# Performance work log

Measured on AMD Instinct MI355X. Metric: run time of the kernel, lower is better.

The kernel has to match this reference:

```python
import jax, jax.numpy as jnp
import numpy as np

B, L, D, H, UNITS = 64, 1024, 1024, 1024, 1024


def setup_inputs() -> dict:
    key = jax.random.key(0)
    ks = jax.random.split(key, 8)
    s = lambda fan_in: 1.0 / np.sqrt(fan_in)
    return {
        "features": jax.random.normal(ks[0], (B, L, D), jnp.float32),
        "hidden": jax.random.normal(ks[1], (B, H), jnp.float32),
        "W1": jax.random.normal(ks[2], (D, UNITS), jnp.float32) * s(D),
        "b1": jnp.zeros((UNITS,), jnp.float32),
        "W2": jax.random.normal(ks[3], (H, UNITS), jnp.float32) * s(H),
        "b2": jnp.zeros((UNITS,), jnp.float32),
        "V": jax.random.normal(ks[4], (UNITS, 1), jnp.float32) * s(UNITS),
        "bV": jnp.zeros((1,), jnp.float32),
    }


def reference(features, hidden, W1, b1, W2, b2, V, bV):
    # features: [B, L, D], hidden: [B, H]
    proj_f = jnp.einsum("bld,du->blu", features, W1) + b1          # [B, L, U]
    proj_h = (hidden @ W2 + b2)[:, None, :]                         # [B, 1, U]
    score = jnp.tanh(proj_f + proj_h)                               # [B, L, U]
    logits = jnp.einsum("blu,uo->blo", score, V) + bV               # [B, L, 1]
    attention_weights = jax.nn.softmax(logits, axis=1)              # [B, L, 1]
    context_vector = jnp.sum(attention_weights * features, axis=1)  # [B, D]
    return context_vector, attention_weights
```

## Files before the change

### kernel.cpp

```cpp
#include <hip/hip_runtime.h>
#include <hip/hip_bf16.h>
#include <stdint.h>

#define B_ 64
#define L_ 1024
#define D_ 1024
#define U_ 1024
#define M_ (B_ * L_)

__device__ __forceinline__ int swz_k(int k, int row) {
  return (k & ~31) | (((((k >> 3) & 3) ^ ((row >> 1) & 3))) << 3) | (k & 7);
}

typedef __attribute__((ext_vector_type(8))) __bf16 bf16x8;
typedef __attribute__((ext_vector_type(4))) float f32x4;
typedef __attribute__((ext_vector_type(8))) unsigned short u16x8;

__device__ __forceinline__ unsigned short f2bf(float f) {
  unsigned u = __float_as_uint(f);
  unsigned r = (u + 0x7fffu + ((u >> 16) & 1u)) >> 16;
  return (unsigned short)r;
}

__device__ __forceinline__ float bf2f(unsigned short h) {
  return __uint_as_float(((unsigned)h) << 16);
}

__device__ __forceinline__ void async_copy16(const void* gptr, void* ldsptr) {
  __builtin_amdgcn_global_load_lds(
      (const __attribute__((address_space(1))) void*)gptr,
      (__attribute__((address_space(3))) void*)ldsptr,
      16, 0, 0);
}

__global__ __launch_bounds__(256) void convert_f_bf16(
    const float4* __restrict__ src, ushort4* __restrict__ dst) {
  long i = (long)blockIdx.x * 256 + threadIdx.x;
  float4 v = src[i];
  ushort4 o;
  o.x = f2bf(v.x); o.y = f2bf(v.y); o.z = f2bf(v.z); o.w = f2bf(v.w);
  int m = (int)(i >> 8);
  int k4 = (int)(i & 255) << 2;
  int kp = swz_k(k4, m);
  dst[(((long)m << 10) + kp) >> 2] = o;
}

__global__ __launch_bounds__(256) void transpose_w1(
    const float* __restrict__ W1, unsigned short* __restrict__ W1T) {
  __shared__ float tile[32][33];
  int tx = threadIdx.x & 31, ty = threadIdx.x >> 5;
  int u0 = blockIdx.x * 32, k0 = blockIdx.y * 32;
#pragma unroll
  for (int i = ty; i < 32; i += 8) tile[i][tx] = W1[(long)(k0 + i) * U_ + u0 + tx];
  __syncthreads();
#pragma unroll
  for (int i = ty; i < 32; i += 8) {
    int u = u0 + i, k = k0 + tx;
    W1T[(long)u * D_ + swz_k(k, u)] = f2bf(tile[tx][i]);
  }
}

__global__ __launch_bounds__(256) void proj_h_kernel(
    const float* __restrict__ hidden, const float* __restrict__ W2,
    const float* __restrict__ b1, const float* __restrict__ b2,
    float* __restrict__ ph) {
  int u = blockIdx.x * 256 + threadIdx.x;
  int bbase = blockIdx.y * 8;
  int h0 = blockIdx.z * 128;
  float acc[8];
  float bias = (blockIdx.z == 0) ? (b1[u] + b2[u]) : 0.0f;
#pragma unroll
  for (int i = 0; i < 8; ++i) acc[i] = bias;
  for (int h = h0; h < h0 + 128; ++h) {
    float w = W2[(long)h * U_ + u];
#pragma unroll
    for (int i = 0; i < 8; ++i) acc[i] += hidden[(bbase + i) * 1024 + h] * w;
  }
#pragma unroll
  for (int i = 0; i < 8; ++i) atomicAdd(&ph[(bbase + i) * U_ + u], acc[i]);
}

__global__ __launch_bounds__(256, 2) void fused_score_kernel(
    const unsigned short* __restrict__ A,
    const unsigned short* __restrict__ Bt,
    const float* __restrict__ ph,
    const float* __restrict__ V,
    float* __restrict__ logits) {
  __shared__ unsigned short As[128 * 32];
  __shared__ unsigned short Bs[128 * 32];

  const int tid = threadIdx.x;
  const int wave = tid >> 6;
  const int lane = tid & 63;
  const int l15 = lane & 15;
  const int quad = lane >> 4;
  const int wm = wave >> 1;
  const int wn = wave & 1;
  const int xk = (l15 >> 1) & 3;

  const int i = blockIdx.x;
  const int mtile = ((i >> 6) << 3) + (i & 7);
  const int ntile = (i >> 3) & 7;
  const long m0 = (long)mtile * 128;
  const int n0 = ntile * 128;

  const int srow = lane >> 2;
  const int skof = (lane & 3) * 8;
  const int c0 = wave * 2;
  const unsigned short* Ab = A + (m0 + srow) * 1024 + skof;
  const unsigned short* Bb = Bt + ((long)n0 + srow) * 1024 + skof;

  f32x4 acc[4][4];
#pragma unroll
  for (int ii = 0; ii < 4; ++ii)
#pragma unroll
    for (int j = 0; j < 4; ++j) acc[ii][j] = (f32x4){0.f, 0.f, 0.f, 0.f};

  for (int k0 = 0; k0 < 1024; k0 += 32) {
#pragma unroll
    for (int cc = 0; cc < 2; ++cc) {
      const int c = c0 + cc;
      async_copy16(Ab + (long)c * 16 * 1024 + k0, &As[c * 512]);
      async_copy16(Bb + (long)c * 16 * 1024 + k0, &Bs[c * 512]);
    }
    __syncthreads();

    bf16x8 af[4], bf[4];
#pragma unroll
    for (int mi = 0; mi < 4; ++mi)
      af[mi] = *(const bf16x8*)&As[(wm * 64 + mi * 16 + l15) * 32 + ((quad ^ xk) << 3)];
#pragma unroll
    for (int ni = 0; ni < 4; ++ni)
      bf[ni] = *(const bf16x8*)&Bs[(wn * 64 + ni * 16 + l15) * 32 + ((quad ^ xk) << 3)];
#pragma unroll
    for (int mi = 0; mi < 4; ++mi)
#pragma unroll
      for (int ni = 0; ni < 4; ++ni)
        acc[mi][ni] = __builtin_amdgcn_mfma_f32_16x16x32_bf16(
            af[mi], bf[ni], acc[mi][ni], 0, 0, 0);
    __syncthreads();
  }

  const int b = (int)(m0 >> 10);
  float phv[4], vv[4];
#pragma unroll
  for (int ni = 0; ni < 4; ++ni) {
    int u = n0 + wn * 64 + ni * 16 + l15;
    phv[ni] = ph[b * U_ + u];
    vv[ni] = V[u];
  }
#pragma unroll
  for (int mi = 0; mi < 4; ++mi) {
#pragma unroll
    for (int r = 0; r < 4; ++r) {
      float part = 0.f;
#pragma unroll
      for (int ni = 0; ni < 4; ++ni) {
        float s = acc[mi][ni][r] + phv[ni];
        float t = __expf(2.0f * s);
        float th = 1.0f - 2.0f * __builtin_amdgcn_rcpf(t + 1.0f);
        part += th * vv[ni];
      }
      part += __shfl_xor(part, 1, 16);
      part += __shfl_xor(part, 2, 16);
      part += __shfl_xor(part, 4, 16);
      part += __shfl_xor(part, 8, 16);
      if (l15 == 0)
        atomicAdd(&logits[m0 + wm * 64 + mi * 16 + quad * 4 + r], part);
    }
  }
}

__global__ __launch_bounds__(256) void softmax_kernel(
    const float* __restrict__ logits, float* __restrict__ wout) {
  __shared__ float redm[4];
  __shared__ float reds[4];
  int b = blockIdx.x;
  int tid = threadIdx.x;
  int wave = tid >> 6, lane = tid & 63;
  float4 v = *(const float4*)&logits[b * 1024 + tid * 4];
  float m = fmaxf(fmaxf(v.x, v.y), fmaxf(v.z, v.w));
#pragma unroll
  for (int off = 32; off >= 1; off >>= 1) m = fmaxf(m, __shfl_xor(m, off, 64));
  if (lane == 0) redm[wave] = m;
  __syncthreads();
  m = fmaxf(fmaxf(redm[0], redm[1]), fmaxf(redm[2], redm[3]));
  float e0 = __expf(v.x - m), e1 = __expf(v.y - m);
  float e2 = __expf(v.z - m), e3 = __expf(v.w - m);
  float s = e0 + e1 + e2 + e3;
#pragma unroll
  for (int off = 32; off >= 1; off >>= 1) s += __shfl_xor(s, off, 64);
  if (lane == 0) reds[wave] = s;
  __syncthreads();
  s = reds[0] + reds[1] + reds[2] + reds[3];
  float inv = 1.0f / s;
  float4 o = {e0 * inv, e1 * inv, e2 * inv, e3 * inv};
  *(float4*)&wout[b * 1024 + tid * 4] = o;
}

__global__ __launch_bounds__(256) void context_kernel(
    const unsigned short* __restrict__ Fh, const float* __restrict__ wv,
    float* __restrict__ out) {
  int b = blockIdx.x;
  int d4 = threadIdx.x * 4;
  int l0 = blockIdx.y * 128;
  const int hi = d4 & ~31, ch = (d4 >> 3) & 3, off = d4 & 7;
  const unsigned short* fp = Fh + ((long)b * 1024 + l0) * 1024;
  const float* wp = wv + b * 1024 + l0;
  float a0 = 0.f, a1 = 0.f, a2 = 0.f, a3 = 0.f;
#pragma unroll 4
  for (int l = 0; l < 128; ++l) {
    int xr = ((l0 + l) >> 1) & 3;
    ushort4 f = *(const ushort4*)(fp + (long)l * 1024 + hi + ((ch ^ xr) << 3) + off);
    float w = wp[l];
    a0 += w * bf2f(f.x);
    a1 += w * bf2f(f.y);
    a2 += w * bf2f(f.z);
    a3 += w * bf2f(f.w);
  }
  atomicAdd(&out[b * 1024 + d4 + 0], a0);
  atomicAdd(&out[b * 1024 + d4 + 1], a1);
  atomicAdd(&out[b * 1024 + d4 + 2], a2);
  atomicAdd(&out[b * 1024 + d4 + 3], a3);
}

extern "C" void kernel_launch(void* const* d_in, const int* in_sizes, int n_in,
                              void* d_out, int out_size, void* d_ws, size_t ws_size,
                              hipStream_t stream) {
  const float* features = (const float*)d_in[0];
  const float* hidden   = (const float*)d_in[1];
  const float* W1       = (const float*)d_in[2];
  const float* b1       = (const float*)d_in[3];
  const float* W2       = (const float*)d_in[4];
  const float* b2       = (const float*)d_in[5];
  const float* V        = (const float*)d_in[6];

  char* ws = (char*)d_ws;
  unsigned short* Fh  = (unsigned short*)ws;
  unsigned short* W1T = (unsigned short*)(ws + 134217728);
  float* ph     = (float*)(ws + 134217728 + 2097152);
  float* logits = (float*)(ws + 134217728 + 2097152 + 262144);
  float* ctx  = (float*)d_out;
  float* wout = (float*)d_out + 65536;

  hipMemsetAsync(ph, 0, 262144 + 262144, stream);
  hipMemsetAsync(d_out, 0, 65536 * sizeof(float), stream);

  convert_f_bf16<<<65536, 256, 0, stream>>>((const float4*)features, (ushort4*)Fh);
  transpose_w1<<<dim3(32, 32), 256, 0, stream>>>(W1, W1T);
  proj_h_kernel<<<dim3(4, 8, 8), 256, 0, stream>>>(hidden, W2, b1, b2, ph);
  fused_score_kernel<<<4096, 256, 0, stream>>>(Fh, W1T, ph, V, logits);
  softmax_kernel<<<64, 256, 0, stream>>>(logits, wout);
  context_kernel<<<dim3(64, 8), 256, 0, stream>>>(Fh, wout, ctx);
}
```

Baseline: 595.6 us.

## Rewrite score GEMM as 256x256 tile with 4-stage LDS async pipeline

The fused score GEMM moves from 128x128 tiles with 256 threads and one barrier-synced stage per k-step to 256x256 tiles with 512 threads. A 4-buffer LDS ring prefetches two k-steps ahead using global_load_lds, with interleaved partial barriers and s_setprio around the MFMA bursts. The intent is to hide load latency and raise operand reuse. The global swizzle on the bf16 feature and W1T copies is dropped in favour of an XOR swizzle applied during staging, which simplifies the conversion and context kernels. The context kernel grid is doubled, and the large LDS footprint (128KB) limits occupancy.

Result: slower. 607.9 us (+2.1%).

```diff
diff --git a/kernel.cpp b/kernel.cpp
--- a/kernel.cpp
+++ b/kernel.cpp
@@ -8,13 +8,8 @@
 #define U_ 1024
 #define M_ (B_ * L_)
 
-__device__ __forceinline__ int swz_k(int k, int row) {
-  return (k & ~31) | (((((k >> 3) & 3) ^ ((row >> 1) & 3))) << 3) | (k & 7);
-}
-
 typedef __attribute__((ext_vector_type(8))) __bf16 bf16x8;
 typedef __attribute__((ext_vector_type(4))) float f32x4;
-typedef __attribute__((ext_vector_type(8))) unsigned short u16x8;
 
 __device__ __forceinline__ unsigned short f2bf(float f) {
   unsigned u = __float_as_uint(f);
@@ -39,10 +34,7 @@
   float4 v = src[i];
   ushort4 o;
   o.x = f2bf(v.x); o.y = f2bf(v.y); o.z = f2bf(v.z); o.w = f2bf(v.w);
-  int m = (int)(i >> 8);
-  int k4 = (int)(i & 255) << 2;
-  int kp = swz_k(k4, m);
-  dst[(((long)m << 10) + kp) >> 2] = o;
+  dst[i] = o;
 }
 
 __global__ __launch_bounds__(256) void transpose_w1(
@@ -56,7 +48,7 @@
 #pragma unroll
   for (int i = ty; i < 32; i += 8) {
     int u = u0 + i, k = k0 + tx;
-    W1T[(long)u * D_ + swz_k(k, u)] = f2bf(tile[tx][i]);
+    W1T[(long)u * D_ + k] = f2bf(tile[tx][i]);
   }
 }
 
@@ -80,93 +72,143 @@
   for (int i = 0; i < 8; ++i) atomicAdd(&ph[(bbase + i) * U_ + u], acc[i]);
 }
 
-__global__ __launch_bounds__(256, 2) void fused_score_kernel(
+#define LDA(rb, i) (*(const bf16x8*)&S[(rb) + arow + (i)*512])
+#define LDB(rb, j) (*(const bf16x8*)&S[(rb) + 8192 + brow + (j)*512])
+#define MM(i, j)                                                  \
+  acc[i][j] = __builtin_amdgcn_mfma_f32_16x16x32_bf16(af[i], bf[j], \
+                                                      acc[i][j], 0, 0, 0)
+#define SYNC_MAIN \
+  asm volatile("s_waitcnt vmcnt(4)" ::: "memory"); __builtin_amdgcn_s_barrier()
+#define SYNC_LAST \
+  asm volatile("s_waitcnt vmcnt(0)" ::: "memory"); __builtin_amdgcn_s_barrier()
+#define SYNC_NONE ((void)0)
+
+#define WINDOW(WT, DO_STAGE, ENDSYNC)                                          \
+  {                                                                            \
+    const int rb = ((WT) & 3) << 14;                                           \
+    const int sb = (((WT) + 2) & 3) << 14;                                     \
+    const int sk = ((WT) + 2) << 5;                                            \
+    bf16x8 af[8], bf[4];                                                       \
+                                                          \
+    if (DO_STAGE) async_copy16(a0 + sk, &S[sb + (wave << 9)]);                 \
+    af[0] = LDA(rb, 0); af[1] = LDA(rb, 1);                                    \
+    af[2] = LDA(rb, 2); af[3] = LDA(rb, 3);                                    \
+    bf[0] = LDB(rb, 0); bf[1] = LDB(rb, 1);                                    \
+    __builtin_amdgcn_s_setprio(1);                                             \
+    MM(0, 0); MM(0, 1); MM(1, 0); MM(1, 1);                                    \
+    MM(2, 0); MM(2, 1); MM(3, 0); MM(3, 1);                                    \
+    __builtin_amdgcn_s_setprio(0);                                             \
+    __builtin_amdgcn_s_barrier();                                              \
+                                                          \
+    if (DO_STAGE) async_copy16(a1 + sk, &S[sb + 4096 + (wave << 9)]);          \
+    bf[2] = LDB(rb, 2); bf[3] = LDB(rb, 3);                                    \
+    __builtin_amdgcn_s_setprio(1);                                             \
+    MM(0, 2); MM(0, 3); MM(1, 2); MM(1, 3);                                    \
+    MM(2, 2); MM(2, 3); MM(3, 2); MM(3, 3);                                    \
+    __builtin_amdgcn_s_setprio(0);                                             \
+    __builtin_amdgcn_s_barrier();                                              \
+                                                          \
+    if (DO_STAGE) async_copy16(b0 + sk, &S[sb + 8192 + (wave << 9)]);          \
+    af[4] = LDA(rb, 4); af[5] = LDA(rb, 5);                                    \
+    af[6] = LDA(rb, 6); af[7] = LDA(rb, 7);                                    \
+    __builtin_amdgcn_s_setprio(1);                                             \
+    MM(4, 0); MM(4, 1); MM(5, 0); MM(5, 1);                                    \
+    MM(6, 0); MM(6, 1); MM(7, 0); MM(7, 1);                                    \
+    __builtin_amdgcn_s_setprio(0);                                             \
+    __builtin_amdgcn_s_barrier();                                              \
+                                                          \
+    if (DO_STAGE) async_copy16(b1 + sk, &S[sb + 12288 + (wave << 9)]);         \
+    __builtin_amdgcn_s_setprio(1);                                             \
+    MM(4, 2); MM(4, 3); MM(5, 2); MM(5, 3);                                    \
+    MM(6, 2); MM(6, 3); MM(7, 2); MM(7, 3);                                    \
+    __builtin_amdgcn_s_setprio(0);                                             \
+    ENDSYNC;                                                                   \
+  }
+
+__global__ __launch_bounds__(512, 2) void fused_score_kernel(
     const unsigned short* __restrict__ A,
     const unsigned short* __restrict__ Bt,
     const float* __restrict__ ph,
     const float* __restrict__ V,
     float* __restrict__ logits) {
-  __shared__ unsigned short As[128 * 32];
-  __shared__ unsigned short Bs[128 * 32];
+  __shared__ unsigned short S[65536];
 
   const int tid = threadIdx.x;
   const int wave = tid >> 6;
   const int lane = tid & 63;
   const int l15 = lane & 15;
   const int quad = lane >> 4;
-  const int wm = wave >> 1;
-  const int wn = wave & 1;
-  const int xk = (l15 >> 1) & 3;
-
-  const int i = blockIdx.x;
-  const int mtile = ((i >> 6) << 3) + (i & 7);
-  const int ntile = (i >> 3) & 7;
-  const long m0 = (long)mtile * 128;
-  const int n0 = ntile * 128;
-
-  const int srow = lane >> 2;
-  const int skof = (lane & 3) * 8;
-  const int c0 = wave * 2;
-  const unsigned short* Ab = A + (m0 + srow) * 1024 + skof;
-  const unsigned short* Bb = Bt + ((long)n0 + srow) * 1024 + skof;
-
-  f32x4 acc[4][4];
-#pragma unroll
-  for (int ii = 0; ii < 4; ++ii)
-#pragma unroll
-    for (int j = 0; j < 4; ++j) acc[ii][j] = (f32x4){0.f, 0.f, 0.f, 0.f};
-
-  for (int k0 = 0; k0 < 1024; k0 += 32) {
-#pragma unroll
-    for (int cc = 0; cc < 2; ++cc) {
-      const int c = c0 + cc;
-      async_copy16(Ab + (long)c * 16 * 1024 + k0, &As[c * 512]);
-      async_copy16(Bb + (long)c * 16 * 1024 + k0, &Bs[c * 512]);
-    }
-    __syncthreads();
-
-    bf16x8 af[4], bf[4];
-#pragma unroll
-    for (int mi = 0; mi < 4; ++mi)
-      af[mi] = *(const bf16x8*)&As[(wm * 64 + mi * 16 + l15) * 32 + ((quad ^ xk) << 3)];
-#pragma unroll
-    for (int ni = 0; ni < 4; ++ni)
-      bf[ni] = *(const bf16x8*)&Bs[(wn * 64 + ni * 16 + l15) * 32 + ((quad ^ xk) << 3)];
-#pragma unroll
-    for (int mi = 0; mi < 4; ++mi)
-#pragma unroll
-      for (int ni = 0; ni < 4; ++ni)
-        acc[mi][ni] = __builtin_amdgcn_mfma_f32_16x16x32_bf16(
-            af[mi], bf[ni], acc[mi][ni], 0, 0, 0);
-    __syncthreads();
-  }
+  const int wm = wave >> 2;
+  const int wn = wave & 3;
+
+  const int bid = blockIdx.x;
+  const int wg = (bid & 7) * 128 + (bid >> 3);
+  const int mtile = wg >> 2;
+  const int ntile = wg & 3;
+  const long m0 = (long)mtile * 256;
+  const int n0 = ntile * 256;
+
+  const int srow = (wave << 4) + (lane >> 2);
+  const int skel = ((lane & 3) << 3) ^ ((lane & 32) ? 16 : 0);
+  const unsigned short* a0 = A + (m0 + srow) * 1024 + skel;
+  const unsigned short* a1 = A + (m0 + 128 + srow) * 1024 + skel;
+  const unsigned short* b0 = Bt + ((long)n0 + srow) * 1024 + skel;
+  const unsigned short* b1 = Bt + ((long)n0 + 128 + srow) * 1024 + skel;
+
+  const int xorq = ((quad * 8) ^ ((l15 & 8) << 1));
+  const int arow = (wm * 128 + l15) * 32 + xorq;
+  const int brow = (wn * 64 + l15) * 32 + xorq;
+
+  f32x4 acc[8][4];
+#pragma unroll
+  for (int i = 0; i < 8; ++i)
+#pragma unroll
+    for (int j = 0; j < 4; ++j) acc[i][j] = (f32x4){0.f, 0.f, 0.f, 0.f};
+
+#pragma unroll
+  for (int t = 0; t < 2; ++t) {
+    const int sbase = t << 14;
+    async_copy16(a0 + t * 32, &S[sbase + (wave << 9)]);
+    async_copy16(a1 + t * 32, &S[sbase + 4096 + (wave << 9)]);
+    async_copy16(b0 + t * 32, &S[sbase + 8192 + (wave << 9)]);
+    async_copy16(b1 + t * 32, &S[sbase + 12288 + (wave << 9)]);
+  }
+  asm volatile("s_waitcnt vmcnt(4)" ::: "memory");
+  __builtin_amdgcn_s_barrier();
+
+#pragma unroll 1
+  for (int t = 0; t < 30; ++t) {
+    WINDOW(t, 1, SYNC_MAIN)
+  }
+  WINDOW(30, 0, SYNC_LAST)
+  WINDOW(31, 0, SYNC_NONE)
 
   const int b = (int)(m0 >> 10);
   float phv[4], vv[4];
 #pragma unroll
-  for (int ni = 0; ni < 4; ++ni) {
-    int u = n0 + wn * 64 + ni * 16 + l15;
-    phv[ni] = ph[b * U_ + u];
-    vv[ni] = V[u];
-  }
-#pragma unroll
-  for (int mi = 0; mi < 4; ++mi) {
+  for (int j = 0; j < 4; ++j) {
+    int u = n0 + wn * 64 + j * 16 + l15;
+    phv[j] = ph[b * U_ + u];
+    vv[j] = V[u];
+  }
+#pragma unroll
+  for (int i = 0; i < 8; ++i) {
 #pragma unroll
     for (int r = 0; r < 4; ++r) {
       float part = 0.f;
 #pragma unroll
-      for (int ni = 0; ni < 4; ++ni) {
-        float s = acc[mi][ni][r] + phv[ni];
-        float t = __expf(2.0f * s);
-        float th = 1.0f - 2.0f * __builtin_amdgcn_rcpf(t + 1.0f);
-        part += th * vv[ni];
+      for (int j = 0; j < 4; ++j) {
+        float s = acc[i][j][r] + phv[j];
+        float e = __expf(2.0f * s);
+        float th = 1.0f - 2.0f * __builtin_amdgcn_rcpf(e + 1.0f);
+        part += th * vv[j];
       }
       part += __shfl_xor(part, 1, 16);
       part += __shfl_xor(part, 2, 16);
       part += __shfl_xor(part, 4, 16);
       part += __shfl_xor(part, 8, 16);
       if (l15 == 0)
-        atomicAdd(&logits[m0 + wm * 64 + mi * 16 + quad * 4 + r], part);
+        atomicAdd(&logits[m0 + wm * 128 + i * 16 + quad * 4 + r], part);
     }
   }
 }
@@ -203,15 +245,13 @@
     float* __restrict__ out) {
   int b = blockIdx.x;
   int d4 = threadIdx.x * 4;
-  int l0 = blockIdx.y * 128;
-  const int hi = d4 & ~31, ch = (d4 >> 3) & 3, off = d4 & 7;
+  int l0 = blockIdx.y * 64;
   const unsigned short* fp = Fh + ((long)b * 1024 + l0) * 1024;
   const float* wp = wv + b * 1024 + l0;
   float a0 = 0.f, a1 = 0.f, a2 = 0.f, a3 = 0.f;
 #pragma unroll 4
-  for (int l = 0; l < 128; ++l) {
-    int xr = ((l0 + l) >> 1) & 3;
-    ushort4 f = *(const ushort4*)(fp + (long)l * 1024 + hi + ((ch ^ xr) << 3) + off);
+  for (int l = 0; l < 64; ++l) {
+    ushort4 f = *(const ushort4*)(fp + (long)l * 1024 + d4);
     float w = wp[l];
     a0 += w * bf2f(f.x);
     a1 += w * bf2f(f.y);
@@ -249,7 +289,7 @@
   convert_f_bf16<<<65536, 256, 0, stream>>>((const float4*)features, (ushort4*)Fh);
   transpose_w1<<<dim3(32, 32), 256, 0, stream>>>(W1, W1T);
   proj_h_kernel<<<dim3(4, 8, 8), 256, 0, stream>>>(hidden, W2, b1, b2, ph);
-  fused_score_kernel<<<4096, 256, 0, stream>>>(Fh, W1T, ph, V, logits);
+  fused_score_kernel<<<1024, 512, 0, stream>>>(Fh, W1T, ph, V, logits);
   softmax_kernel<<<64, 256, 0, stream>>>(logits, wout);
-  context_kernel<<<dim3(64, 8), 256, 0, stream>>>(Fh, wout, ctx);
-}
+  context_kernel<<<dim3(64, 16), 256, 0, stream>>>(Fh, wout, ctx);
+}
```
